# Optimization experiments

Hardware: AMD Instinct MI355X
Metric: run time of the kernel (lower is better)

## Reference

```python
import jax, jax.numpy as jnp
import numpy as np

N_NODES = 16384
HID_IN = 1024   # hid_size (GCN in/out dim)
HID_MID = 1500  # hidden_size
N_EDGES = 131072


def setup_inputs() -> dict:
    key = jax.random.key(0)
    k1, k2, k3, k4, k5, k6 = jax.random.split(key, 6)
    x = jax.random.normal(k1, (N_NODES, HID_IN), dtype=jnp.float32)
    edge_index = jax.random.randint(k2, (2, N_EDGES), 0, N_NODES, dtype=jnp.int64)
    # GCNConv weights (glorot-ish scale) and biases
    W1 = jax.random.normal(k3, (HID_IN, HID_MID), dtype=jnp.float32) / np.sqrt(HID_IN)
    b1 = jnp.zeros((HID_MID,), dtype=jnp.float32)
    W2 = jax.random.normal(k4, (HID_MID, HID_IN), dtype=jnp.float32) / np.sqrt(HID_MID)
    b2 = jnp.zeros((HID_IN,), dtype=jnp.float32)
    return {"x": x, "edge_index": edge_index, "W1": W1, "b1": b1, "W2": W2, "b2": b2}


def _gcn_conv(x, W, b, src, dst, inv_sqrt_deg, n_nodes):
    # PyG GCNConv: out[i] = sum_{(j->i)} d_j^{-1/2} d_i^{-1/2} (x W)[j] + b
    h = x @ W                                   # [N, out]
    norm = inv_sqrt_deg[src] * inv_sqrt_deg[dst]  # [E]
    msg = h[src] * norm[:, None]                 # gather + scale [E, out]
    out = jax.ops.segment_sum(msg, dst, num_segments=n_nodes)
    return out + b


def reference(x, edge_index, W1, b1, W2, b2):
    n = x.shape[0]
    # add self-loops (GCNConv default)
    loops = jnp.arange(n, dtype=edge_index.dtype)
    src = jnp.concatenate([edge_index[0], loops])
    dst = jnp.concatenate([edge_index[1], loops])
    deg = jax.ops.segment_sum(jnp.ones_like(dst, dtype=x.dtype), dst, num_segments=n)
    inv_sqrt_deg = jnp.where(deg > 0, jax.lax.rsqrt(jnp.maximum(deg, 1.0)), 0.0)
    h = _gcn_conv(x, W1, b1, src, dst, inv_sqrt_deg, n)
    h = jax.nn.relu(h)  # dropout skipped (eval mode)
    out = _gcn_conv(h, W2, b2, src, dst, inv_sqrt_deg, n)
    return out
```

## Files before the change

kernel.cpp:

```cpp
#include <hip/hip_runtime.h>
#include <cstdint>
#include <cstddef>

#define NN 16384
#define DIN 1024
#define DMID 1500
#define DMIDP 1536
#define NE 131072

typedef __bf16 bf16;
typedef __bf16 bf16x4 __attribute__((ext_vector_type(4)));
typedef __bf16 bf16x8 __attribute__((ext_vector_type(8)));
typedef float f32x4 __attribute__((ext_vector_type(4)));

#define GLOBAL_AS __attribute__((address_space(1)))
#define LDS_AS __attribute__((address_space(3)))

__device__ __forceinline__ void gload_lds16(const bf16* g, bf16* l) {
    __builtin_amdgcn_global_load_lds((GLOBAL_AS const unsigned int*)(g),
                                     (LDS_AS unsigned int*)(l), 16, 0, 0);
}

__global__ void k_zero_cnt(int* cnt) {
    cnt[blockIdx.x * 256 + threadIdx.x] = 0;
}

__global__ void k_count(const int* __restrict__ dst, int* cnt) {
    int e = blockIdx.x * 256 + threadIdx.x;
    atomicAdd(&cnt[dst[e]], 1);
}

__global__ __launch_bounds__(1024) void k_scan(const int* __restrict__ cnt,
                                               int* __restrict__ rowptr,
                                               int* __restrict__ cursor,
                                               float* __restrict__ isd) {
    __shared__ int sums[1024];
    int t = threadIdx.x;
    int base = t * 16;
    int v[16];
    int s = 0;
#pragma unroll
    for (int k = 0; k < 16; ++k) { v[k] = cnt[base + k]; s += v[k]; }
    sums[t] = s;
    __syncthreads();
    for (int off = 1; off < 1024; off <<= 1) {
        int y = (t >= off) ? sums[t - off] : 0;
        __syncthreads();
        sums[t] += y;
        __syncthreads();
    }
    int run = sums[t] - s;
#pragma unroll
    for (int k = 0; k < 16; ++k) {
        rowptr[base + k] = run;
        cursor[base + k] = run;
        isd[base + k] = rsqrtf((float)(v[k] + 1));
        run += v[k];
    }
    if (t == 1023) rowptr[NN] = run;
}

__global__ void k_fill(const int* __restrict__ src, const int* __restrict__ dst,
                       int* cursor, const float* __restrict__ isd,
                       int* __restrict__ csr_src, float* __restrict__ csr_w) {
    int e = blockIdx.x * 256 + threadIdx.x;
    int s = src[e], d = dst[e];
    int pos = atomicAdd(&cursor[d], 1);
    csr_src[pos] = s;
    csr_w[pos] = isd[s] * isd[d];
}

__global__ void k_cvt_x(const float4* __restrict__ x, bf16x4* __restrict__ xb) {
    int i = blockIdx.x * 256 + threadIdx.x;
    float4 v = x[i];
    bf16x4 o;
    o[0] = (bf16)v.x; o[1] = (bf16)v.y; o[2] = (bf16)v.z; o[3] = (bf16)v.w;
    xb[i] = o;
}

__global__ void k_cvt_w1(const float* __restrict__ W1, bf16* __restrict__ W1b) {
    int n = blockIdx.x;
    for (int k = threadIdx.x; k < DIN; k += 256)
        W1b[n * DIN + k] = (n < DMID) ? (bf16)W1[(size_t)k * DMID + n] : (bf16)0.0f;
}

__global__ void k_cvt_w2(const float* __restrict__ W2, bf16* __restrict__ W2b) {
    int n = blockIdx.x;
    for (int k = threadIdx.x; k < DMIDP; k += 256)
        W2b[n * DMIDP + k] = (k < DMID) ? (bf16)W2[(size_t)k * DIN + n] : (bf16)0.0f;
}

template <bool RELU_BIAS>
__global__ __launch_bounds__(256) void gemm_bt(const bf16* __restrict__ A,
                                               const bf16* __restrict__ Bt,
                                               bf16* __restrict__ C,
                                               const float* __restrict__ bias,
                                               int M, int N, int K) {
    __shared__ __align__(16) bf16 sA[128 * 64];
    __shared__ __align__(16) bf16 sB[128 * 64];
    const int tid = threadIdx.x;
    const int wid = tid >> 6;
    const int lane = tid & 63;
    const int bn = blockIdx.x;
    const int bm = blockIdx.y;

    const int ldrow = (wid << 5) + (lane >> 3);
    const int ldcol = (lane & 7) << 3;
    const size_t aG = (size_t)(bm * 128 + ldrow) * K + ldcol;
    const size_t bG = (size_t)(bn * 128 + ldrow) * K + ldcol;
    bf16* sAw = sA + (wid << 5) * 64;
    bf16* sBw = sB + (wid << 5) * 64;

    const int wm = (wid & 1) << 6;
    const int wn = (wid >> 1) << 6;
    const int fr = lane & 15;
    const int fq = lane >> 4;

    f32x4 acc[4][4];
#pragma unroll
    for (int i = 0; i < 4; ++i)
#pragma unroll
        for (int j = 0; j < 4; ++j) acc[i][j] = {0.f, 0.f, 0.f, 0.f};

    for (int k0 = 0; k0 < K; k0 += 64) {
#pragma unroll
        for (int i = 0; i < 4; ++i)
            gload_lds16(A + aG + (size_t)(8 * i) * K + k0, sAw + i * 512);
#pragma unroll
        for (int i = 0; i < 4; ++i)
            gload_lds16(Bt + bG + (size_t)(8 * i) * K + k0, sBw + i * 512);
        __syncthreads();
#pragma unroll
        for (int s = 0; s < 2; ++s) {
            bf16x8 af[4], bf_[4];
#pragma unroll
            for (int mt = 0; mt < 4; ++mt)
                af[mt] = *(const bf16x8*)&sA[(wm + mt * 16 + fr) * 64 + s * 32 + fq * 8];
#pragma unroll
            for (int nt = 0; nt < 4; ++nt)
                bf_[nt] = *(const bf16x8*)&sB[(wn + nt * 16 + fr) * 64 + s * 32 + fq * 8];
#pragma unroll
            for (int mt = 0; mt < 4; ++mt)
#pragma unroll
                for (int nt = 0; nt < 4; ++nt)
                    acc[mt][nt] = __builtin_amdgcn_mfma_f32_16x16x32_bf16(
                        af[mt], bf_[nt], acc[mt][nt], 0, 0, 0);
        }
        __syncthreads();
    }

#pragma unroll
    for (int nt = 0; nt < 4; ++nt) {
        int col = bn * 128 + wn + nt * 16 + fr;
        float b = 0.0f;
        if (RELU_BIAS) b = (col < DMID) ? bias[col] : 0.0f;
#pragma unroll
        for (int mt = 0; mt < 4; ++mt) {
            int row0 = bm * 128 + wm + mt * 16 + fq * 4;
#pragma unroll
            for (int r = 0; r < 4; ++r) {
                float v = acc[mt][nt][r];
                if (RELU_BIAS) v = fmaxf(v + b, 0.0f);
                C[(size_t)(row0 + r) * N + col] = (bf16)v;
            }
        }
    }
}

#define CHUNK 64

__global__ __launch_bounds__(128) void k_aggX(const bf16* __restrict__ X,
                                              const int* __restrict__ rowptr,
                                              const int* __restrict__ csr_src,
                                              const float* __restrict__ csr_w,
                                              const float* __restrict__ isd,
                                              bf16* __restrict__ XA) {
    __shared__ int sj[CHUNK];
    __shared__ float sw[CHUNK];
    int i = blockIdx.x;
    int t = threadIdx.x;
    int c0 = t * 8;
    int beg = rowptr[i], end = rowptr[i + 1];
    float wi = isd[i];
    float w0 = wi * wi;
    float a[8];
    bf16x8 h = *(const bf16x8*)&X[(size_t)i * DIN + c0];
#pragma unroll
    for (int k = 0; k < 8; ++k) a[k] = w0 * (float)h[k];
    for (int c = beg; c < end; c += CHUNK) {
        int n = end - c; if (n > CHUNK) n = CHUNK;
        if (t < n) { sj[t] = csr_src[c + t]; sw[t] = csr_w[c + t]; }
        __syncthreads();
        int e = 0;
        for (; e + 1 < n; e += 2) {
            float wa = sw[e], wb = sw[e + 1];
            bf16x8 ha = *(const bf16x8*)&X[(size_t)sj[e] * DIN + c0];
            bf16x8 hb = *(const bf16x8*)&X[(size_t)sj[e + 1] * DIN + c0];
#pragma unroll
            for (int k = 0; k < 8; ++k) a[k] += wa * (float)ha[k];
#pragma unroll
            for (int k = 0; k < 8; ++k) a[k] += wb * (float)hb[k];
        }
        if (e < n) {
            float wa = sw[e];
            bf16x8 ha = *(const bf16x8*)&X[(size_t)sj[e] * DIN + c0];
#pragma unroll
            for (int k = 0; k < 8; ++k) a[k] += wa * (float)ha[k];
        }
        __syncthreads();
    }
    bf16x8 o;
#pragma unroll
    for (int k = 0; k < 8; ++k) o[k] = (bf16)a[k];
    *(bf16x8*)&XA[(size_t)i * DIN + c0] = o;
}

__global__ __launch_bounds__(128) void k_agg2(const bf16* __restrict__ H,
                                              const int* __restrict__ rowptr,
                                              const int* __restrict__ csr_src,
                                              const float* __restrict__ csr_w,
                                              const float* __restrict__ isd,
                                              const float* __restrict__ b2,
                                              float* __restrict__ out) {
    __shared__ int sj[CHUNK];
    __shared__ float sw[CHUNK];
    int i = blockIdx.x;
    int t = threadIdx.x;
    int c0 = t * 8;
    int beg = rowptr[i], end = rowptr[i + 1];
    float wi = isd[i];
    float w0 = wi * wi;
    float a[8];
    bf16x8 h = *(const bf16x8*)&H[(size_t)i * DIN + c0];
#pragma unroll
    for (int k = 0; k < 8; ++k) a[k] = w0 * (float)h[k];
    for (int c = beg; c < end; c += CHUNK) {
        int n = end - c; if (n > CHUNK) n = CHUNK;
        if (t < n) { sj[t] = csr_src[c + t]; sw[t] = csr_w[c + t]; }
        __syncthreads();
        int e = 0;
        for (; e + 1 < n; e += 2) {
            float wa = sw[e], wb = sw[e + 1];
            bf16x8 ha = *(const bf16x8*)&H[(size_t)sj[e] * DIN + c0];
            bf16x8 hb = *(const bf16x8*)&H[(size_t)sj[e + 1] * DIN + c0];
#pragma unroll
            for (int k = 0; k < 8; ++k) a[k] += wa * (float)ha[k];
#pragma unroll
            for (int k = 0; k < 8; ++k) a[k] += wb * (float)hb[k];
        }
        if (e < n) {
            float wa = sw[e];
            bf16x8 ha = *(const bf16x8*)&H[(size_t)sj[e] * DIN + c0];
#pragma unroll
            for (int k = 0; k < 8; ++k) a[k] += wa * (float)ha[k];
        }
        __syncthreads();
    }
    float4 o0, o1;
    o0.x = a[0] + b2[c0 + 0]; o0.y = a[1] + b2[c0 + 1];
    o0.z = a[2] + b2[c0 + 2]; o0.w = a[3] + b2[c0 + 3];
    o1.x = a[4] + b2[c0 + 4]; o1.y = a[5] + b2[c0 + 5];
    o1.z = a[6] + b2[c0 + 6]; o1.w = a[7] + b2[c0 + 7];
    *(float4*)&out[(size_t)i * DIN + c0] = o0;
    *(float4*)&out[(size_t)i * DIN + c0 + 4] = o1;
}

extern "C" void kernel_launch(void* const* d_in, const int* in_sizes, int n_in,
                              void* d_out, int out_size, void* d_ws, size_t ws_size,
                              hipStream_t stream) {
    const float* x = (const float*)d_in[0];
    const int* ei = (const int*)d_in[1];
    const float* W1 = (const float*)d_in[2];
    const float* b1 = (const float*)d_in[3];
    const float* W2 = (const float*)d_in[4];
    const float* b2 = (const float*)d_in[5];
    float* out = (float*)d_out;
    const int* src = ei;
    const int* dst = ei + NE;

    char* ws = (char*)d_ws;
    int* cnt      = (int*)(ws + 0);
    int* cursor   = (int*)(ws + 65536);
    float* isd    = (float*)(ws + 131072);
    int* rowptr   = (int*)(ws + 196608);
    int* csr_src  = (int*)(ws + 263168);
    float* csr_w  = (float*)(ws + 787456);
    bf16* Xb      = (bf16*)(ws + 1311744);
    bf16* XA      = (bf16*)(ws + 34866176);
    bf16* W1b     = (bf16*)(ws + 68420608);
    bf16* W2b     = (bf16*)(ws + 71566336);
    bf16* Y1b     = (bf16*)(ws + 74712064);
    bf16* H2b     = XA;

    k_zero_cnt<<<NN / 256, 256, 0, stream>>>(cnt);
    k_count<<<NE / 256, 256, 0, stream>>>(dst, cnt);
    k_scan<<<1, 1024, 0, stream>>>(cnt, rowptr, cursor, isd);
    k_fill<<<NE / 256, 256, 0, stream>>>(src, dst, cursor, isd, csr_src, csr_w);

    k_cvt_x<<<NN * DIN / 4 / 256, 256, 0, stream>>>((const float4*)x, (bf16x4*)Xb);
    k_cvt_w1<<<DMIDP, 256, 0, stream>>>(W1, W1b);
    k_cvt_w2<<<DIN, 256, 0, stream>>>(W2, W2b);

    k_aggX<<<NN, 128, 0, stream>>>(Xb, rowptr, csr_src, csr_w, isd, XA);
    dim3 g1(DMIDP / 128, NN / 128);
    gemm_bt<true><<<g1, 256, 0, stream>>>(XA, W1b, Y1b, b1, NN, DMIDP, DIN);

    dim3 g2(DIN / 128, NN / 128);
    gemm_bt<false><<<g2, 256, 0, stream>>>(Y1b, W2b, H2b, nullptr, NN, DIN, DMIDP);
    k_agg2<<<NN, 128, 0, stream>>>(H2b, rowptr, csr_src, csr_w, isd, b2, out);
}
```

Measured before the change: 436.0 us.

## Pad CSR rows to multiples of four and unroll aggregation without LDS staging

Each node's CSR segment is padded to a multiple of four with zero-weight self edges, so the aggregation kernels can read four neighbours per iteration straight from global memory with no shared-memory staging or barriers. This exposes more independent gathers per thread and removes the syncthreads overhead. The GEMM grid is also transposed so consecutive blocks walk M instead of N, which changes how tiles share the L2 cache. The cost is an extra padding kernel, larger CSR buffers, and up to three wasted zero-weight gathers per node.

```diff
diff --git a/kernel.cpp b/kernel.cpp
--- a/kernel.cpp
+++ b/kernel.cpp
@@ -37,10 +37,14 @@
     __shared__ int sums[1024];
     int t = threadIdx.x;
     int base = t * 16;
-    int v[16];
+    int v[16], p[16];
     int s = 0;
 #pragma unroll
-    for (int k = 0; k < 16; ++k) { v[k] = cnt[base + k]; s += v[k]; }
+    for (int k = 0; k < 16; ++k) {
+        v[k] = cnt[base + k];
+        p[k] = (v[k] + 3) & ~3;
+        s += p[k];
+    }
     sums[t] = s;
     __syncthreads();
     for (int off = 1; off < 1024; off <<= 1) {
@@ -55,7 +59,7 @@
         rowptr[base + k] = run;
         cursor[base + k] = run;
         isd[base + k] = rsqrtf((float)(v[k] + 1));
-        run += v[k];
+        run += p[k];
     }
     if (t == 1023) rowptr[NN] = run;
 }
@@ -68,6 +72,18 @@
     int pos = atomicAdd(&cursor[d], 1);
     csr_src[pos] = s;
     csr_w[pos] = isd[s] * isd[d];
+}
+
+__global__ void k_pad(const int* __restrict__ cnt, const int* __restrict__ rowptr,
+                      int* __restrict__ csr_src, float* __restrict__ csr_w) {
+    int i = blockIdx.x * 256 + threadIdx.x;
+    int c = cnt[i];
+    int p = (c + 3) & ~3;
+    int base = rowptr[i];
+    for (int q = c; q < p; ++q) {
+        csr_src[base + q] = i;
+        csr_w[base + q] = 0.0f;
+    }
 }
 
 __global__ void k_cvt_x(const float4* __restrict__ x, bf16x4* __restrict__ xb) {
@@ -101,8 +117,8 @@
     const int tid = threadIdx.x;
     const int wid = tid >> 6;
     const int lane = tid & 63;
-    const int bn = blockIdx.x;
-    const int bm = blockIdx.y;
+    const int bm = blockIdx.x;
+    const int bn = blockIdx.y;
 
     const int ldrow = (wid << 5) + (lane >> 3);
     const int ldcol = (lane & 7) << 3;
@@ -167,7 +183,6 @@
     }
 }
 
-#define CHUNK 64
 
 __global__ __launch_bounds__(128) void k_aggX(const bf16* __restrict__ X,
                                               const int* __restrict__ rowptr,
@@ -175,8 +190,6 @@
                                               const float* __restrict__ csr_w,
                                               const float* __restrict__ isd,
                                               bf16* __restrict__ XA) {
-    __shared__ int sj[CHUNK];
-    __shared__ float sw[CHUNK];
     int i = blockIdx.x;
     int t = threadIdx.x;
     int c0 = t * 8;
@@ -187,27 +200,23 @@
     bf16x8 h = *(const bf16x8*)&X[(size_t)i * DIN + c0];
 #pragma unroll
     for (int k = 0; k < 8; ++k) a[k] = w0 * (float)h[k];
-    for (int c = beg; c < end; c += CHUNK) {
-        int n = end - c; if (n > CHUNK) n = CHUNK;
-        if (t < n) { sj[t] = csr_src[c + t]; sw[t] = csr_w[c + t]; }
-        __syncthreads();
-        int e = 0;
-        for (; e + 1 < n; e += 2) {
-            float wa = sw[e], wb = sw[e + 1];
-            bf16x8 ha = *(const bf16x8*)&X[(size_t)sj[e] * DIN + c0];
-            bf16x8 hb = *(const bf16x8*)&X[(size_t)sj[e + 1] * DIN + c0];
-#pragma unroll
-            for (int k = 0; k < 8; ++k) a[k] += wa * (float)ha[k];
-#pragma unroll
-            for (int k = 0; k < 8; ++k) a[k] += wb * (float)hb[k];
-        }
-        if (e < n) {
-            float wa = sw[e];
-            bf16x8 ha = *(const bf16x8*)&X[(size_t)sj[e] * DIN + c0];
-#pragma unroll
-            for (int k = 0; k < 8; ++k) a[k] += wa * (float)ha[k];
-        }
-        __syncthreads();
+    for (int e = beg; e < end; e += 4) {
+        int j0 = csr_src[e + 0], j1 = csr_src[e + 1];
+        int j2 = csr_src[e + 2], j3 = csr_src[e + 3];
+        float wa = csr_w[e + 0], wb = csr_w[e + 1];
+        float wc = csr_w[e + 2], wd = csr_w[e + 3];
+        bf16x8 h0 = *(const bf16x8*)&X[(size_t)j0 * DIN + c0];
+        bf16x8 h1 = *(const bf16x8*)&X[(size_t)j1 * DIN + c0];
+        bf16x8 h2 = *(const bf16x8*)&X[(size_t)j2 * DIN + c0];
+        bf16x8 h3 = *(const bf16x8*)&X[(size_t)j3 * DIN + c0];
+#pragma unroll
+        for (int k = 0; k < 8; ++k) a[k] += wa * (float)h0[k];
+#pragma unroll
+        for (int k = 0; k < 8; ++k) a[k] += wb * (float)h1[k];
+#pragma unroll
+        for (int k = 0; k < 8; ++k) a[k] += wc * (float)h2[k];
+#pragma unroll
+        for (int k = 0; k < 8; ++k) a[k] += wd * (float)h3[k];
     }
     bf16x8 o;
 #pragma unroll
@@ -222,8 +231,6 @@
                                               const float* __restrict__ isd,
                                               const float* __restrict__ b2,
                                               float* __restrict__ out) {
-    __shared__ int sj[CHUNK];
-    __shared__ float sw[CHUNK];
     int i = blockIdx.x;
     int t = threadIdx.x;
     int c0 = t * 8;
@@ -234,27 +241,23 @@
     bf16x8 h = *(const bf16x8*)&H[(size_t)i * DIN + c0];
 #pragma unroll
     for (int k = 0; k < 8; ++k) a[k] = w0 * (float)h[k];
-    for (int c = beg; c < end; c += CHUNK) {
-        int n = end - c; if (n > CHUNK) n = CHUNK;
-        if (t < n) { sj[t] = csr_src[c + t]; sw[t] = csr_w[c + t]; }
-        __syncthreads();
-        int e = 0;
-        for (; e + 1 < n; e += 2) {
-            float wa = sw[e], wb = sw[e + 1];
-            bf16x8 ha = *(const bf16x8*)&H[(size_t)sj[e] * DIN + c0];
-            bf16x8 hb = *(const bf16x8*)&H[(size_t)sj[e + 1] * DIN + c0];
-#pragma unroll
-            for (int k = 0; k < 8; ++k) a[k] += wa * (float)ha[k];
-#pragma unroll
-            for (int k = 0; k < 8; ++k) a[k] += wb * (float)hb[k];
-        }
-        if (e < n) {
-            float wa = sw[e];
-            bf16x8 ha = *(const bf16x8*)&H[(size_t)sj[e] * DIN + c0];
-#pragma unroll
-            for (int k = 0; k < 8; ++k) a[k] += wa * (float)ha[k];
-        }
-        __syncthreads();
+    for (int e = beg; e < end; e += 4) {
+        int j0 = csr_src[e + 0], j1 = csr_src[e + 1];
+        int j2 = csr_src[e + 2], j3 = csr_src[e + 3];
+        float wa = csr_w[e + 0], wb = csr_w[e + 1];
+        float wc = csr_w[e + 2], wd = csr_w[e + 3];
+        bf16x8 h0 = *(const bf16x8*)&H[(size_t)j0 * DIN + c0];
+        bf16x8 h1 = *(const bf16x8*)&H[(size_t)j1 * DIN + c0];
+        bf16x8 h2 = *(const bf16x8*)&H[(size_t)j2 * DIN + c0];
+        bf16x8 h3 = *(const bf16x8*)&H[(size_t)j3 * DIN + c0];
+#pragma unroll
+        for (int k = 0; k < 8; ++k) a[k] += wa * (float)h0[k];
+#pragma unroll
+        for (int k = 0; k < 8; ++k) a[k] += wb * (float)h1[k];
+#pragma unroll
+        for (int k = 0; k < 8; ++k) a[k] += wc * (float)h2[k];
+#pragma unroll
+        for (int k = 0; k < 8; ++k) a[k] += wd * (float)h3[k];
     }
     float4 o0, o1;
     o0.x = a[0] + b2[c0 + 0]; o0.y = a[1] + b2[c0 + 1];
@@ -283,29 +286,30 @@
     int* cursor   = (int*)(ws + 65536);
     float* isd    = (float*)(ws + 131072);
     int* rowptr   = (int*)(ws + 196608);
-    int* csr_src  = (int*)(ws + 263168);
-    float* csr_w  = (float*)(ws + 787456);
-    bf16* Xb      = (bf16*)(ws + 1311744);
-    bf16* XA      = (bf16*)(ws + 34866176);
-    bf16* W1b     = (bf16*)(ws + 68420608);
-    bf16* W2b     = (bf16*)(ws + 71566336);
-    bf16* Y1b     = (bf16*)(ws + 74712064);
+    int* csr_src  = (int*)(ws + 327680);
+    float* csr_w  = (float*)(ws + 1376256);
+    bf16* Xb      = (bf16*)(ws + 2424832);
+    bf16* XA      = (bf16*)(ws + 35979264);
+    bf16* W1b     = (bf16*)(ws + 69533696);
+    bf16* W2b     = (bf16*)(ws + 72679424);
+    bf16* Y1b     = (bf16*)(ws + 75825152);
     bf16* H2b     = XA;
 
     k_zero_cnt<<<NN / 256, 256, 0, stream>>>(cnt);
     k_count<<<NE / 256, 256, 0, stream>>>(dst, cnt);
     k_scan<<<1, 1024, 0, stream>>>(cnt, rowptr, cursor, isd);
     k_fill<<<NE / 256, 256, 0, stream>>>(src, dst, cursor, isd, csr_src, csr_w);
+    k_pad<<<NN / 256, 256, 0, stream>>>(cnt, rowptr, csr_src, csr_w);
 
     k_cvt_x<<<NN * DIN / 4 / 256, 256, 0, stream>>>((const float4*)x, (bf16x4*)Xb);
     k_cvt_w1<<<DMIDP, 256, 0, stream>>>(W1, W1b);
     k_cvt_w2<<<DIN, 256, 0, stream>>>(W2, W2b);
 
     k_aggX<<<NN, 128, 0, stream>>>(Xb, rowptr, csr_src, csr_w, isd, XA);
-    dim3 g1(DMIDP / 128, NN / 128);
+    dim3 g1(NN / 128, DMIDP / 128);
     gemm_bt<true><<<g1, 256, 0, stream>>>(XA, W1b, Y1b, b1, NN, DMIDP, DIN);
 
-    dim3 g2(DIN / 128, NN / 128);
+    dim3 g2(NN / 128, DIN / 128);
     gemm_bt<false><<<g2, 256, 0, stream>>>(Y1b, W2b, H2b, nullptr, NN, DIN, DMIDP);
     k_agg2<<<NN, 128, 0, stream>>>(H2b, rowptr, csr_src, csr_w, isd, b2, out);
 }
```

After: 442.5 us. No clear change (+1.5%).
